# Optimization experiments

Hardware: AMD Instinct MI355X
Metric: run time of the kernel (lower is better)

The kernel has to match this reference:

```python
import jax, jax.numpy as jnp
import numpy as np

N, E, F_IN, H = 10000, 20000, 128, 8
C1, C2 = 512, 256          # per-head channels: head_dim1*8, head_dim2*8
B, OUT = 64, 10            # graphs per batch, output_dim


def _lin(k, fi, fo):
    return (jax.random.normal(k, (fi, fo), jnp.float32) / np.sqrt(fi)).astype(jnp.float32)


def setup_inputs() -> dict:
    key = jax.random.key(0)
    ks = jax.random.split(key, 24)
    inp = {
        "x": jax.random.normal(ks[0], (N, F_IN), jnp.float32),
        "edge_index": jax.random.randint(ks[1], (2, E), 0, N),
        "batch": jnp.sort(jax.random.randint(ks[2], (N,), 0, B)),
        # conv1 (in=F_IN, per-head C1, H heads)
        "Wq1": _lin(ks[3], F_IN, H * C1), "bq1": 0.01 * jax.random.normal(ks[4], (H * C1,)),
        "Wk1": _lin(ks[5], F_IN, H * C1), "bk1": 0.01 * jax.random.normal(ks[6], (H * C1,)),
        "Wv1": _lin(ks[7], F_IN, H * C1), "bv1": 0.01 * jax.random.normal(ks[8], (H * C1,)),
        "Ws1": _lin(ks[9], F_IN, C1), "bs1": 0.01 * jax.random.normal(ks[10], (C1,)),
        # conv2 (in=C1, per-head C2)
        "Wq2": _lin(ks[11], C1, H * C2), "bq2": 0.01 * jax.random.normal(ks[12], (H * C2,)),
        "Wk2": _lin(ks[13], C1, H * C2), "bk2": 0.01 * jax.random.normal(ks[14], (H * C2,)),
        "Wv2": _lin(ks[15], C1, H * C2), "bv2": 0.01 * jax.random.normal(ks[16], (H * C2,)),
        "Ws2": _lin(ks[17], C1, C2), "bs2": 0.01 * jax.random.normal(ks[18], (C2,)),
        # GlobalAttention gate and final fc
        "Wg": _lin(ks[19], C2, 1), "bg": jnp.zeros((1,), jnp.float32),
        "Wf": _lin(ks[20], C2, OUT), "bf": 0.01 * jax.random.normal(ks[21], (OUT,)),
    }
    return inp


def _segment_softmax(alpha, idx, n):
    # numerically-stable softmax over variable-size segments (PyG softmax)
    amax = jax.ops.segment_max(alpha, idx, num_segments=n)
    amax = jnp.where(jnp.isfinite(amax), amax, 0.0)
    e = jnp.exp(alpha - amax[idx])
    denom = jax.ops.segment_sum(e, idx, num_segments=n)
    return e / (denom[idx] + 1e-16)


def _transformer_conv(x, edge_index, Wq, bq, Wk, bk, Wv, bv, Ws, bs, C):
    n = x.shape[0]
    src, dst = edge_index[0], edge_index[1]  # message flows src -> dst
    q = (x @ Wq + bq).reshape(n, H, C)
    k = (x @ Wk + bk).reshape(n, H, C)
    v = (x @ Wv + bv).reshape(n, H, C)
    # per-edge multi-head attention logits [E, H]
    alpha = jnp.einsum('ehc,ehc->eh', q[dst], k[src]) / np.sqrt(C).astype(np.float32)
    a = _segment_softmax(alpha, dst, n)                       # [E, H]
    out = jax.ops.segment_sum(a[:, :, None] * v[src], dst, num_segments=n)  # [N, H, C]
    out = out.mean(axis=1)                                    # concat=False -> head mean
    return out + x @ Ws + bs                                  # root/skip connection


def reference(x, edge_index, batch,
              Wq1, bq1, Wk1, bk1, Wv1, bv1, Ws1, bs1,
              Wq2, bq2, Wk2, bk2, Wv2, bv2, Ws2, bs2,
              Wg, bg, Wf, bf):
    h = jax.nn.elu(_transformer_conv(x, edge_index, Wq1, bq1, Wk1, bk1, Wv1, bv1, Ws1, bs1, C1))
    h = jax.nn.elu(_transformer_conv(h, edge_index, Wq2, bq2, Wk2, bk2, Wv2, bv2, Ws2, bs2, C2))
    # GlobalAttention pooling: gate softmax within each graph, weighted sum
    gate = _segment_softmax((h @ Wg + bg)[:, 0], batch, B)    # [N]
    g = jax.ops.segment_sum(gate[:, None] * h, batch, num_segments=B)  # [B, C2]
    return g @ Wf + bf
```

## Files before the change

### kernel.cpp

```cpp
#include <hip/hip_runtime.h>
#include <math.h>

#define NN 10000
#define NE 20000
#define FIN 128
#define NHEAD 8
#define C1 512
#define C2 256
#define NB 64
#define NOUT 10

typedef _Float16 half8v __attribute__((ext_vector_type(8)));
typedef _Float16 half4v __attribute__((ext_vector_type(4)));
typedef _Float16 half2v __attribute__((ext_vector_type(2)));
typedef float f32x4 __attribute__((ext_vector_type(4)));

template<int VEC> struct VecT;
template<> struct VecT<2> { using T = half2v; };
template<> struct VecT<4> { using T = half4v; };
template<> struct VecT<8> { using T = half8v; };

__device__ __forceinline__ unsigned enc_f(float f) {
    unsigned u = __float_as_uint(f);
    return (u & 0x80000000u) ? ~u : (u | 0x80000000u);
}
__device__ __forceinline__ float dec_f(unsigned e) {
    return (e & 0x80000000u) ? __uint_as_float(e & 0x7fffffffu) : __uint_as_float(~e);
}

__device__ __forceinline__ void gload16(const _Float16* g, _Float16* l) {
    __builtin_amdgcn_global_load_lds(
        (const __attribute__((address_space(1))) unsigned int*)(const void*)g,
        (__attribute__((address_space(3))) unsigned int*)(void*)l, 16, 0, 0);
}

__global__ void cvt_f16(const float* __restrict__ in, _Float16* __restrict__ out, int n) {
    int i = blockIdx.x * blockDim.x + threadIdx.x;
    if (i < n) out[i] = (_Float16)in[i];
}

__global__ void transpose_cvt(const float* __restrict__ W, _Float16* __restrict__ Wt,
                              int K, int N) {
    __shared__ float tile[32][33];
    int n0 = blockIdx.x * 32, k0 = blockIdx.y * 32;
    int tx = threadIdx.x, ty = threadIdx.y;
    for (int j = ty; j < 32; j += 8) tile[j][tx] = W[(size_t)(k0 + j) * N + n0 + tx];
    __syncthreads();
    for (int j = ty; j < 32; j += 8)
        Wt[(size_t)(n0 + j) * K + k0 + tx] = (_Float16)tile[tx][j];
}

__global__ void transpose_stack(const float* __restrict__ Wv, _Float16* __restrict__ Bt,
                                int Cin, int Cout) {
    __shared__ float tile[32][33];
    int h = blockIdx.z;
    int c0 = blockIdx.x * 32, k0 = blockIdx.y * 32;
    int tx = threadIdx.x, ty = threadIdx.y;
    for (int j = ty; j < 32; j += 8)
        tile[j][tx] = Wv[(size_t)(k0 + j) * (NHEAD * Cout) + (size_t)h * Cout + c0 + tx];
    __syncthreads();
    for (int j = ty; j < 32; j += 8)
        Bt[(size_t)(c0 + j) * (NHEAD * Cin) + (size_t)h * Cin + k0 + tx] = (_Float16)tile[tx][j];
}

__global__ void bvmean_k(const float* __restrict__ bv, float* __restrict__ bvm, int C) {
    int c = blockIdx.x * blockDim.x + threadIdx.x;
    if (c >= C) return;
    float s = 0.f;
    #pragma unroll
    for (int h = 0; h < NHEAD; ++h) s += bv[h * C + c];
    bvm[c] = s * (1.0f / NHEAD);
}

__global__ void concat_bias3(const float* __restrict__ a, const float* __restrict__ b,
                             const float* __restrict__ c, float* __restrict__ o) {
    int i = blockIdx.x * blockDim.x + threadIdx.x;
    const int n = NHEAD * C2;
    if (i < n) o[i] = a[i];
    else if (i < 2 * n) o[i] = b[i - n];
    else if (i < 3 * n) o[i] = c[i - 2 * n];
}

__global__ void mstack_k(const _Float16* __restrict__ wtq1, const _Float16* __restrict__ wtk1,
                         _Float16* __restrict__ Mst) {
    int h = blockIdx.z;
    int i = blockIdx.x * 16 + threadIdx.x;
    int j = blockIdx.y * 16 + threadIdx.y;
    float acc = 0.f;
    for (int c = 0; c < C1; ++c)
        acc += (float)wtq1[((size_t)h * C1 + c) * FIN + i] *
               (float)wtk1[((size_t)h * C1 + c) * FIN + j];
    Mst[((size_t)h * FIN + j) * FIN + i] = (_Float16)acc;
}

__global__ void uvprep(const float* __restrict__ Wq1, const float* __restrict__ Wk1,
                       const float* __restrict__ bq1, const float* __restrict__ bk1,
                       float* __restrict__ u, float* __restrict__ v, float* __restrict__ ch) {
    int h = blockIdx.x, i = threadIdx.x;
    float su = 0.f, sv = 0.f;
    for (int c = 0; c < C1; ++c) {
        su += Wq1[(size_t)i * (NHEAD * C1) + h * C1 + c] * bk1[h * C1 + c];
        sv += Wk1[(size_t)i * (NHEAD * C1) + h * C1 + c] * bq1[h * C1 + c];
    }
    u[h * FIN + i] = su;
    v[h * FIN + i] = sv;
    if (i == 0) {
        float s = 0.f;
        for (int c = 0; c < C1; ++c) s += bq1[h * C1 + c] * bk1[h * C1 + c];
        ch[h] = s;
    }
}

__global__ void udvs_k(const _Float16* __restrict__ xb, const float* __restrict__ u,
                       const float* __restrict__ v, const float* __restrict__ ch,
                       float* __restrict__ ud, float* __restrict__ vs) {
    int idx = blockIdx.x * blockDim.x + threadIdx.x;
    if (idx >= NN * NHEAD) return;
    int n = idx >> 3, h = idx & 7;
    float su = ch[h], sv = 0.f;
    for (int i = 0; i < FIN; ++i) {
        float xv = (float)xb[(size_t)n * FIN + i];
        su += xv * u[h * FIN + i];
        sv += xv * v[h * FIN + i];
    }
    ud[idx] = su;
    vs[idx] = sv;
}

template<bool OUT_HALF, bool ACCUM>
__global__ __launch_bounds__(256) void gemm_tn(
    const _Float16* __restrict__ A, const _Float16* __restrict__ Bt,
    const float* __restrict__ bias, void* __restrict__ Cout, int ldc,
    int M, int K)
{
    __shared__ _Float16 As[128 * 32];
    __shared__ _Float16 Bs[128 * 32];
    const int t = threadIdx.x;
    const int m0 = blockIdx.y * 128, n0 = blockIdx.x * 128;
    const int w = t >> 6, lane = t & 63;
    const int wr = w >> 1, wc = w & 1;
    const int r_lo = lane >> 2, slot = lane & 3;

    f32x4 acc[4][4];
    #pragma unroll
    for (int m = 0; m < 4; ++m)
        #pragma unroll
        for (int n = 0; n < 4; ++n)
            #pragma unroll
            for (int j = 0; j < 4; ++j) acc[m][n][j] = 0.f;

    for (int k0 = 0; k0 < K; k0 += 32) {
        #pragma unroll
        for (int i = 0; i < 2; ++i) {
            int chunk = 2 * w + i;
            int row = chunk * 16 + r_lo;
            int gr = m0 + row; gr = gr < M ? gr : M - 1;
            gload16(A + (size_t)gr * K + k0 + slot * 8, &As[chunk * 512]);
            gload16(Bt + (size_t)(n0 + row) * K + k0 + slot * 8, &Bs[chunk * 512]);
        }
        __syncthreads();
        half8v af[4], bf[4];
        #pragma unroll
        for (int m = 0; m < 4; ++m)
            af[m] = *(const half8v*)(&As[(wr * 64 + m * 16 + (lane & 15)) * 32 + (lane >> 4) * 8]);
        #pragma unroll
        for (int n = 0; n < 4; ++n)
            bf[n] = *(const half8v*)(&Bs[(wc * 64 + n * 16 + (lane & 15)) * 32 + (lane >> 4) * 8]);
        #pragma unroll
        for (int m = 0; m < 4; ++m)
            #pragma unroll
            for (int n = 0; n < 4; ++n)
                acc[m][n] = __builtin_amdgcn_mfma_f32_16x16x32_f16(af[m], bf[n], acc[m][n], 0, 0, 0);
        __syncthreads();
    }
    #pragma unroll
    for (int m = 0; m < 4; ++m) {
        int r0 = m0 + wr * 64 + m * 16 + (lane >> 4) * 4;
        #pragma unroll
        for (int n = 0; n < 4; ++n) {
            int col = n0 + wc * 64 + n * 16 + (lane & 15);
            float b = 0.f;
            if (!ACCUM) b = bias[col];
            #pragma unroll
            for (int r = 0; r < 4; ++r) {
                int row = r0 + r;
                if (row < M) {
                    float v = acc[m][n][r] + b;
                    if (ACCUM) v += ((float*)Cout)[(size_t)row * ldc + col];
                    if (OUT_HALF) ((_Float16*)Cout)[(size_t)row * ldc + col] = (_Float16)v;
                    else          ((float*)Cout)[(size_t)row * ldc + col] = v;
                }
            }
        }
    }
}

__global__ void zero_i32(int* __restrict__ p, int n) {
    int i = blockIdx.x * blockDim.x + threadIdx.x;
    if (i < n) p[i] = 0;
}
__global__ void hist_dst(const int* __restrict__ dst, int* __restrict__ deg) {
    int e = blockIdx.x * blockDim.x + threadIdx.x;
    if (e < NE) atomicAdd(&deg[dst[e]], 1);
}
__global__ void scan_deg(const int* __restrict__ deg, int* __restrict__ rowptr,
                         int* __restrict__ cursor, int n) {
    __shared__ int s[256];
    __shared__ int carry;
    int t = threadIdx.x;
    if (t == 0) carry = 0;
    __syncthreads();
    for (int base = 0; base < n; base += 256) {
        int v = (base + t < n) ? deg[base + t] : 0;
        s[t] = v;
        __syncthreads();
        for (int off = 1; off < 256; off <<= 1) {
            int x = (t >= off) ? s[t - off] : 0;
            __syncthreads();
            s[t] += x;
            __syncthreads();
        }
        int excl = carry + s[t] - v;
        if (base + t < n) { rowptr[base + t] = excl; cursor[base + t] = excl; }
        __syncthreads();
        if (t == 255) carry += s[255];
        __syncthreads();
    }
    if (t == 0) rowptr[n] = carry;
}
__global__ void scatter_edges(const int* __restrict__ dst, int* __restrict__ cursor,
                              int* __restrict__ eids) {
    int e = blockIdx.x * blockDim.x + threadIdx.x;
    if (e < NE) {
        int pos = atomicAdd(&cursor[dst[e]], 1);
        eids[pos] = e;
    }
}

__global__ void init_seg(unsigned* __restrict__ amax, float* __restrict__ denom, int n) {
    int i = blockIdx.x * blockDim.x + threadIdx.x;
    if (i < n) { amax[i] = 0x007FFFFFu; denom[i] = 0.f; }
}

__global__ void edge_alpha_lr(const _Float16* __restrict__ T, const _Float16* __restrict__ X,
                              const float* __restrict__ ud, const float* __restrict__ vs,
                              const int* __restrict__ src, const int* __restrict__ dst,
                              float* __restrict__ alpha, unsigned* __restrict__ amaxU,
                              float scale)
{
    int gi = blockIdx.x * blockDim.x + threadIdx.x;
    int e = gi >> 6, lane = threadIdx.x & 63;
    if (e >= NE) return;
    int s = src[e], d = dst[e];
    half2v xv = *(const half2v*)(X + (size_t)s * FIN + lane * 2);
    #pragma unroll
    for (int h = 0; h < NHEAD; ++h) {
        half2v tv = *(const half2v*)(T + ((size_t)d * NHEAD + h) * FIN + lane * 2);
        float sum = (float)tv[0] * (float)xv[0] + (float)tv[1] * (float)xv[1];
        #pragma unroll
        for (int off = 32; off; off >>= 1) sum += __shfl_xor(sum, off);
        if (lane == 0) {
            float al = (sum + ud[(size_t)d * NHEAD + h] + vs[(size_t)s * NHEAD + h]) * scale;
            alpha[(size_t)e * NHEAD + h] = al;
            atomicMax(&amaxU[(size_t)d * NHEAD + h], enc_f(al));
        }
    }
}

template<int C>
__global__ void edge_alpha_f(const _Float16* __restrict__ Q, const _Float16* __restrict__ Kh,
                             int ldq, const int* __restrict__ src, const int* __restrict__ dst,
                             float* __restrict__ alpha, unsigned* __restrict__ amaxU,
                             float scale, int hbase, int G)
{
    constexpr int VEC = C / 64;
    using vecH = typename VecT<VEC>::T;
    int gi = blockIdx.x * blockDim.x + threadIdx.x;
    int e = gi >> 6, lane = threadIdx.x & 63;
    if (e >= NE) return;
    int s = src[e], d = dst[e];
    const _Float16* qp = Q + (size_t)d * ldq + lane * VEC;
    const _Float16* kp = Kh + (size_t)s * ldq + lane * VEC;
    for (int h = 0; h < G; ++h) {
        vecH q = *(const vecH*)(qp + h * C);
        vecH k = *(const vecH*)(kp + h * C);
        float sum = 0.f;
        #pragma unroll
        for (int j = 0; j < VEC; ++j) sum += (float)q[j] * (float)k[j];
        #pragma unroll
        for (int off = 32; off; off >>= 1) sum += __shfl_xor(sum, off);
        if (lane == 0) {
            float al = sum * scale;
            alpha[(size_t)e * NHEAD + hbase + h] = al;
            atomicMax(&amaxU[(size_t)d * NHEAD + hbase + h], enc_f(al));
        }
    }
}

__global__ void edge_expsum(const float* __restrict__ alpha, const int* __restrict__ dst,
                            const unsigned* __restrict__ amaxU,
                            float* __restrict__ ev, float* __restrict__ denom)
{
    int i = blockIdx.x * blockDim.x + threadIdx.x;
    if (i >= NE * NHEAD) return;
    int e = i >> 3, h = i & 7;
    int d = dst[e];
    float ex = expf(alpha[i] - dec_f(amaxU[(size_t)d * NHEAD + h]));
    ev[i] = ex;
    atomicAdd(&denom[(size_t)d * NHEAD + h], ex);
}

template<int C, int G>
__global__ void zaccum(const _Float16* __restrict__ X, const float* __restrict__ ev,
                       const float* __restrict__ denom, const int* __restrict__ rowptr,
                       const int* __restrict__ eids, const int* __restrict__ src,
                       _Float16* __restrict__ Z, int hbase)
{
    constexpr int VEC = C / 64;
    using vecH = typename VecT<VEC>::T;
    int gi = blockIdx.x * blockDim.x + threadIdx.x;
    int n = gi >> 6, lane = threadIdx.x & 63;
    if (n >= NN) return;
    int beg = rowptr[n], end = rowptr[n + 1];
    float rd[G];
    #pragma unroll
    for (int h = 0; h < G; ++h)
        rd[h] = (1.0f / NHEAD) / (denom[(size_t)n * NHEAD + hbase + h] + 1e-16f);
    float acc[G][VEC];
    #pragma unroll
    for (int h = 0; h < G; ++h)
        #pragma unroll
        for (int j = 0; j < VEC; ++j) acc[h][j] = 0.f;
    for (int i = beg; i < end; ++i) {
        int e = eids[i];
        int s = src[e];
        vecH xv = *(const vecH*)(X + (size_t)s * C + lane * VEC);
        #pragma unroll
        for (int h = 0; h < G; ++h) {
            float cf = ev[(size_t)e * NHEAD + hbase + h] * rd[h];
            #pragma unroll
            for (int j = 0; j < VEC; ++j) acc[h][j] += cf * (float)xv[j];
        }
    }
    #pragma unroll
    for (int h = 0; h < G; ++h) {
        vecH o;
        #pragma unroll
        for (int j = 0; j < VEC; ++j) o[j] = (_Float16)acc[h][j];
        *(vecH*)(Z + (size_t)n * (G * C) + (size_t)h * C + lane * VEC) = o;
    }
}

template<int C>
__global__ void node_aggr(const _Float16* __restrict__ V, int ldv,
                          const float* __restrict__ ev, const float* __restrict__ denom,
                          const int* __restrict__ rowptr, const int* __restrict__ eids,
                          const int* __restrict__ src, float* __restrict__ acc,
                          int hbase, int G)
{
    constexpr int VEC = C / 64;
    using vecH = typename VecT<VEC>::T;
    int gi = blockIdx.x * blockDim.x + threadIdx.x;
    int n = gi >> 6, lane = threadIdx.x & 63;
    if (n >= NN) return;
    int beg = rowptr[n], end = rowptr[n + 1];
    float a[VEC];
    #pragma unroll
    for (int j = 0; j < VEC; ++j) a[j] = 0.f;
    for (int h = 0; h < G; ++h) {
        float rd = 1.f / (denom[(size_t)n * NHEAD + hbase + h] + 1e-16f) * (1.f / NHEAD);
        for (int i = beg; i < end; ++i) {
            int e = eids[i];
            int s = src[e];
            float coeff = ev[(size_t)e * NHEAD + hbase + h] * rd;
            vecH v = *(const vecH*)(V + (size_t)s * ldv + h * C + lane * VEC);
            #pragma unroll
            for (int j = 0; j < VEC; ++j) a[j] += coeff * (float)v[j];
        }
    }
    float* ap = acc + (size_t)n * C + lane * VEC;
    #pragma unroll
    for (int j = 0; j < VEC; ++j) ap[j] += a[j];
}

__global__ void elu_k(float* __restrict__ x, int n) {
    int i = blockIdx.x * blockDim.x + threadIdx.x;
    if (i < n) { float v = x[i]; x[i] = v > 0.f ? v : expm1f(v); }
}
__global__ void elu_cvt_bias(const float* __restrict__ in, _Float16* __restrict__ out,
                             const float* __restrict__ bvm, const int* __restrict__ deg,
                             int total) {
    int i = blockIdx.x * blockDim.x + threadIdx.x;
    if (i >= total) return;
    int c = i & (C1 - 1), n = i >> 9;
    float v = in[i] + (deg[n] > 0 ? bvm[c] : 0.f);
    v = v > 0.f ? v : expm1f(v);
    out[i] = (_Float16)v;
}

__global__ __launch_bounds__(256) void pool_fused(
    const float* __restrict__ H2, const float* __restrict__ Wg,
    const float* __restrict__ bg, const int* __restrict__ batch,
    const float* __restrict__ Wf, const float* __restrict__ bf,
    float* __restrict__ glogit, float* __restrict__ out)
{
    const int b = blockIdx.x;
    const int t = threadIdx.x, lane = t & 63, w = t >> 6;
    __shared__ int sbeg, send;
    __shared__ float sred[4];
    if (t == 0) {
        int lo = 0, hi = NN;
        while (lo < hi) { int mid = (lo + hi) >> 1; if (batch[mid] < b) lo = mid + 1; else hi = mid; }
        sbeg = lo;
        hi = NN;
        while (lo < hi) { int mid = (lo + hi) >> 1; if (batch[mid] < b + 1) lo = mid + 1; else hi = mid; }
        send = lo;
    }
    __syncthreads();
    const int beg = sbeg, end = send;
    const float bg0 = bg[0];

    float lmax = -INFINITY;
    for (int n = beg + w; n < end; n += 4) {
        float4 h = ((const float4*)(H2 + (size_t)n * C2))[lane];
        float4 wv = ((const float4*)Wg)[lane];
        float sum = h.x * wv.x + h.y * wv.y + h.z * wv.z + h.w * wv.w;
        #pragma unroll
        for (int off = 32; off; off >>= 1) sum += __shfl_xor(sum, off);
        sum += bg0;
        if (lane == 0) glogit[n] = sum;
        lmax = fmaxf(lmax, sum);
    }
    if (lane == 0) sred[w] = lmax;
    __syncthreads();
    float m = fmaxf(fmaxf(sred[0], sred[1]), fmaxf(sred[2], sred[3]));
    if (!isfinite(m)) m = 0.f;
    __syncthreads();

    float ls = 0.f;
    for (int n = beg + t; n < end; n += 256) {
        float e = expf(glogit[n] - m);
        glogit[n] = e;
        ls += e;
    }
    #pragma unroll
    for (int off = 32; off; off >>= 1) ls += __shfl_xor(ls, off);
    if (lane == 0) sred[w] = ls;
    __syncthreads();
    const float denom = sred[0] + sred[1] + sred[2] + sred[3] + 1e-16f;
    __syncthreads();

    float acc = 0.f;
    for (int n = beg; n < end; ++n)
        acc += glogit[n] * H2[(size_t)n * C2 + t];
    const float gc = acc / denom;

    for (int o = 0; o < NOUT; ++o) {
        float p = gc * Wf[t * NOUT + o];
        #pragma unroll
        for (int off = 32; off; off >>= 1) p += __shfl_xor(p, off);
        __syncthreads();
        if (lane == 0) sred[w] = p;
        __syncthreads();
        if (t == 0) out[b * NOUT + o] = sred[0] + sred[1] + sred[2] + sred[3] + bf[o];
    }
}

extern "C" void kernel_launch(void* const* d_in, const int* in_sizes, int n_in,
                              void* d_out, int out_size, void* d_ws, size_t ws_size,
                              hipStream_t stream) {
    (void)in_sizes; (void)n_in; (void)out_size; (void)ws_size;
    const float* x     = (const float*)d_in[0];
    const int*   ei    = (const int*)  d_in[1];
    const int*   batch = (const int*)  d_in[2];
    const float* Wq1 = (const float*)d_in[3];  const float* bq1 = (const float*)d_in[4];
    const float* Wk1 = (const float*)d_in[5];  const float* bk1 = (const float*)d_in[6];
    const float* Wv1 = (const float*)d_in[7];  const float* bv1 = (const float*)d_in[8];
    const float* Ws1 = (const float*)d_in[9];  const float* bs1 = (const float*)d_in[10];
    const float* Wq2 = (const float*)d_in[11]; const float* bq2 = (const float*)d_in[12];
    const float* Wk2 = (const float*)d_in[13]; const float* bk2 = (const float*)d_in[14];
    const float* Wv2 = (const float*)d_in[15]; const float* bv2 = (const float*)d_in[16];
    const float* Ws2 = (const float*)d_in[17]; const float* bs2 = (const float*)d_in[18];
    const float* Wg  = (const float*)d_in[19]; const float* bg  = (const float*)d_in[20];
    const float* Wf  = (const float*)d_in[21]; const float* bf  = (const float*)d_in[22];

    const int* src = ei;
    const int* dst = ei + NE;

    char* base = (char*)d_ws;
    size_t off = 0;
    auto alloc = [&](size_t bytes) -> char* {
        char* p = base + off;
        off = (off + bytes + 255) & ~(size_t)255;
        return p;
    };
    _Float16* xb    = (_Float16*)alloc((size_t)NN * FIN * 2);
    _Float16* wtq1  = (_Float16*)alloc((size_t)NHEAD * C1 * FIN * 2);
    _Float16* wtk1  = (_Float16*)alloc((size_t)NHEAD * C1 * FIN * 2);
    _Float16* bvs1  = (_Float16*)alloc((size_t)C1 * NHEAD * FIN * 2);
    _Float16* wts1  = (_Float16*)alloc((size_t)C1 * FIN * 2);
    _Float16* wqkv2 = (_Float16*)alloc((size_t)3 * NHEAD * C2 * C1 * 2);
    _Float16* wts2  = (_Float16*)alloc((size_t)C2 * C1 * 2);
    _Float16* Mst   = (_Float16*)alloc((size_t)NHEAD * FIN * FIN * 2);
    float* uvecs = (float*)alloc((size_t)NHEAD * FIN * 4);
    float* vvecs = (float*)alloc((size_t)NHEAD * FIN * 4);
    float* chd   = (float*)alloc((size_t)NHEAD * 4);
    float* ud    = (float*)alloc((size_t)NN * NHEAD * 4);
    float* vs    = (float*)alloc((size_t)NN * NHEAD * 4);
    float* zbias = (float*)alloc((size_t)NHEAD * FIN * 4);
    float* bqkv2 = (float*)alloc((size_t)3 * NHEAD * C2 * 4);
    float* acc1  = (float*)alloc((size_t)NN * C1 * 4);
    _Float16* h1b = (_Float16*)alloc((size_t)NN * C1 * 2);
    float* alpha = (float*)alloc((size_t)NE * NHEAD * 4);
    float* ev    = (float*)alloc((size_t)NE * NHEAD * 4);
    unsigned* amaxU = (unsigned*)alloc((size_t)NN * NHEAD * 4);
    float* denom = (float*)alloc((size_t)NN * NHEAD * 4);
    int* deg    = (int*)alloc((size_t)NN * 4);
    int* rowptr = (int*)alloc((size_t)(NN + 1) * 4);
    int* cursor = (int*)alloc((size_t)NN * 4);
    int* eids   = (int*)alloc((size_t)NE * 4);
    float* bvm1 = (float*)alloc((size_t)C1 * 4);
    _Float16* Tbuf   = (_Float16*)alloc((size_t)NN * NHEAD * FIN * 2);
    _Float16* QKVbuf = (_Float16*)alloc((size_t)NN * 3 * NHEAD * C2 * 2);
    _Float16* Zbuf = QKVbuf;
    float* acc2 = acc1;
    const int LDQKV = 3 * NHEAD * C2;

    const dim3 blk(256);
    const float sc1 = 1.0f / sqrtf((float)C1);
    const float sc2 = 1.0f / sqrtf((float)C2);
    const int edge_blocks = (NE * 64) / 256;
    const int node_blocks = (NN * 64) / 256;
    const int gy = (NN + 127) / 128;

    cvt_f16<<<((size_t)NN * FIN + 255) / 256, blk, 0, stream>>>(x, xb, NN * FIN);
    {
        dim3 tb(32, 8);
        transpose_cvt<<<dim3(NHEAD * C1 / 32, FIN / 32), tb, 0, stream>>>(Wq1, wtq1, FIN, NHEAD * C1);
        transpose_cvt<<<dim3(NHEAD * C1 / 32, FIN / 32), tb, 0, stream>>>(Wk1, wtk1, FIN, NHEAD * C1);
        transpose_stack<<<dim3(C1 / 32, FIN / 32, NHEAD), tb, 0, stream>>>(Wv1, bvs1, FIN, C1);
        transpose_cvt<<<dim3(C1 / 32, FIN / 32),         tb, 0, stream>>>(Ws1, wts1, FIN, C1);
        transpose_cvt<<<dim3(NHEAD * C2 / 32, C1 / 32),  tb, 0, stream>>>(Wq2, wqkv2, C1, NHEAD * C2);
        transpose_cvt<<<dim3(NHEAD * C2 / 32, C1 / 32),  tb, 0, stream>>>(
            Wk2, wqkv2 + (size_t)NHEAD * C2 * C1, C1, NHEAD * C2);
        transpose_cvt<<<dim3(NHEAD * C2 / 32, C1 / 32),  tb, 0, stream>>>(
            Wv2, wqkv2 + (size_t)2 * NHEAD * C2 * C1, C1, NHEAD * C2);
        transpose_cvt<<<dim3(C2 / 32, C1 / 32),          tb, 0, stream>>>(Ws2, wts2, C1, C2);
    }
    bvmean_k<<<(C1 + 255) / 256, blk, 0, stream>>>(bv1, bvm1, C1);
    mstack_k<<<dim3(FIN / 16, FIN / 16, NHEAD), dim3(16, 16), 0, stream>>>(wtq1, wtk1, Mst);
    uvprep<<<NHEAD, FIN, 0, stream>>>(Wq1, Wk1, bq1, bk1, uvecs, vvecs, chd);
    udvs_k<<<(NN * NHEAD + 255) / 256, blk, 0, stream>>>(xb, uvecs, vvecs, chd, ud, vs);
    zero_i32<<<(NHEAD * FIN + 255) / 256, blk, 0, stream>>>((int*)zbias, NHEAD * FIN);
    concat_bias3<<<(3 * NHEAD * C2 + 255) / 256, blk, 0, stream>>>(bq2, bk2, bv2, bqkv2);

    zero_i32<<<(NN + 255) / 256, blk, 0, stream>>>(deg, NN);
    hist_dst<<<(NE + 255) / 256, blk, 0, stream>>>(dst, deg);
    scan_deg<<<1, blk, 0, stream>>>(deg, rowptr, cursor, NN);
    scatter_edges<<<(NE + 255) / 256, blk, 0, stream>>>(dst, cursor, eids);

    gemm_tn<true, false><<<dim3(NHEAD * FIN / 128, gy), blk, 0, stream>>>(
        xb, Mst, zbias, Tbuf, NHEAD * FIN, NN, FIN);
    init_seg<<<(NN * NHEAD + 255) / 256, blk, 0, stream>>>(amaxU, denom, NN * NHEAD);
    edge_alpha_lr<<<edge_blocks, blk, 0, stream>>>(Tbuf, xb, ud, vs, src, dst,
                                                   alpha, amaxU, sc1);
    edge_expsum<<<(NE * NHEAD + 255) / 256, blk, 0, stream>>>(alpha, dst, amaxU, ev, denom);
    gemm_tn<false, false><<<dim3(C1 / 128, gy), blk, 0, stream>>>(
        xb, wts1, bs1, acc1, C1, NN, FIN);
    zaccum<FIN, NHEAD><<<node_blocks, blk, 0, stream>>>(xb, ev, denom, rowptr, eids, src,
                                                        Zbuf, 0);
    gemm_tn<false, true><<<dim3(C1 / 128, gy), blk, 0, stream>>>(
        Zbuf, bvs1, nullptr, acc1, C1, NN, NHEAD * FIN);
    elu_cvt_bias<<<((size_t)NN * C1 + 255) / 256, blk, 0, stream>>>(
        acc1, h1b, bvm1, deg, NN * C1);

    gemm_tn<false, false><<<dim3(C2 / 128, gy), blk, 0, stream>>>(
        h1b, wts2, bs2, acc2, C2, NN, C1);
    init_seg<<<(NN * NHEAD + 255) / 256, blk, 0, stream>>>(amaxU, denom, NN * NHEAD);
    gemm_tn<true, false><<<dim3(LDQKV / 128, gy), blk, 0, stream>>>(
        h1b, wqkv2, bqkv2, QKVbuf, LDQKV, NN, C1);
    edge_alpha_f<C2><<<edge_blocks, blk, 0, stream>>>(
        QKVbuf, QKVbuf + NHEAD * C2, LDQKV, src, dst, alpha, amaxU, sc2, 0, NHEAD);
    edge_expsum<<<(NE * NHEAD + 255) / 256, blk, 0, stream>>>(alpha, dst, amaxU, ev, denom);
    node_aggr<C2><<<node_blocks, blk, 0, stream>>>(
        QKVbuf + 2 * NHEAD * C2, LDQKV, ev, denom, rowptr, eids, src, acc2, 0, NHEAD);
    elu_k<<<((size_t)NN * C2 + 255) / 256, blk, 0, stream>>>(acc2, NN * C2);

    pool_fused<<<NB, blk, 0, stream>>>(acc2, Wg, bg, batch, Wf, bf, alpha, (float*)d_out);
}
```

Before: 656.2 us.

## Merge skip GEMMs into QK/QKV GEMMs and add ILP to edge kernels

Concatenates the skip-connection weights onto the attention projection weights, so each layer runs one GEMM over the shared input. A new dual-output epilogue writes half-precision attention columns and fp32 skip columns to separate buffers. Layer-2 edge-logit and node-aggregation kernels now load all heads' vectors up front and iterate edges once with all heads unrolled, rather than looping per head. This removes two kernel launches and re-reads of the input, and adds memory-level parallelism, at the cost of more register pressure.

```diff
diff --git a/kernel.cpp b/kernel.cpp
--- a/kernel.cpp
+++ b/kernel.cpp
@@ -72,13 +72,19 @@
     bvm[c] = s * (1.0f / NHEAD);
 }
 
-__global__ void concat_bias3(const float* __restrict__ a, const float* __restrict__ b,
-                             const float* __restrict__ c, float* __restrict__ o) {
+__global__ void bcat1_k(const float* __restrict__ bs1, float* __restrict__ o) {
+    int i = blockIdx.x * blockDim.x + threadIdx.x;
+    if (i < NHEAD * FIN + C1) o[i] = (i < NHEAD * FIN) ? 0.f : bs1[i - NHEAD * FIN];
+}
+__global__ void bcat2_k(const float* __restrict__ bq2, const float* __restrict__ bk2,
+                        const float* __restrict__ bv2, const float* __restrict__ bs2,
+                        float* __restrict__ o) {
     int i = blockIdx.x * blockDim.x + threadIdx.x;
     const int n = NHEAD * C2;
-    if (i < n) o[i] = a[i];
-    else if (i < 2 * n) o[i] = b[i - n];
-    else if (i < 3 * n) o[i] = c[i - 2 * n];
+    if (i < n) o[i] = bq2[i];
+    else if (i < 2 * n) o[i] = bk2[i - n];
+    else if (i < 3 * n) o[i] = bv2[i - 2 * n];
+    else if (i < 3 * n + C2) o[i] = bs2[i - 3 * n];
 }
 
 __global__ void mstack_k(const _Float16* __restrict__ wtq1, const _Float16* __restrict__ wtk1,
@@ -127,52 +133,53 @@
     vs[idx] = sv;
 }
 
+#define GEMM_BODY                                                                   \
+    __shared__ _Float16 As[128 * 32];                                               \
+    __shared__ _Float16 Bs[128 * 32];                                               \
+    const int t = threadIdx.x;                                                      \
+    const int m0 = blockIdx.y * 128, n0 = blockIdx.x * 128;                         \
+    const int w = t >> 6, lane = t & 63;                                            \
+    const int wr = w >> 1, wc = w & 1;                                              \
+    const int r_lo = lane >> 2, slot = lane & 3;                                    \
+    f32x4 acc[4][4];                                                                \
+    _Pragma("unroll")                                                               \
+    for (int m = 0; m < 4; ++m)                                                     \
+        _Pragma("unroll")                                                           \
+        for (int n = 0; n < 4; ++n)                                                 \
+            _Pragma("unroll")                                                       \
+            for (int j = 0; j < 4; ++j) acc[m][n][j] = 0.f;                         \
+    for (int k0 = 0; k0 < K; k0 += 32) {                                            \
+        _Pragma("unroll")                                                           \
+        for (int i = 0; i < 2; ++i) {                                               \
+            int chunk = 2 * w + i;                                                  \
+            int row = chunk * 16 + r_lo;                                            \
+            int gr = m0 + row; gr = gr < M ? gr : M - 1;                            \
+            gload16(A + (size_t)gr * K + k0 + slot * 8, &As[chunk * 512]);          \
+            gload16(Bt + (size_t)(n0 + row) * K + k0 + slot * 8, &Bs[chunk * 512]); \
+        }                                                                           \
+        __syncthreads();                                                            \
+        half8v af[4], bf[4];                                                        \
+        _Pragma("unroll")                                                           \
+        for (int m = 0; m < 4; ++m)                                                 \
+            af[m] = *(const half8v*)(&As[(wr * 64 + m * 16 + (lane & 15)) * 32 + (lane >> 4) * 8]); \
+        _Pragma("unroll")                                                           \
+        for (int n = 0; n < 4; ++n)                                                 \
+            bf[n] = *(const half8v*)(&Bs[(wc * 64 + n * 16 + (lane & 15)) * 32 + (lane >> 4) * 8]); \
+        _Pragma("unroll")                                                           \
+        for (int m = 0; m < 4; ++m)                                                 \
+            _Pragma("unroll")                                                       \
+            for (int n = 0; n < 4; ++n)                                             \
+                acc[m][n] = __builtin_amdgcn_mfma_f32_16x16x32_f16(af[m], bf[n], acc[m][n], 0, 0, 0); \
+        __syncthreads();                                                            \
+    }
+
 template<bool OUT_HALF, bool ACCUM>
 __global__ __launch_bounds__(256) void gemm_tn(
     const _Float16* __restrict__ A, const _Float16* __restrict__ Bt,
     const float* __restrict__ bias, void* __restrict__ Cout, int ldc,
     int M, int K)
 {
-    __shared__ _Float16 As[128 * 32];
-    __shared__ _Float16 Bs[128 * 32];
-    const int t = threadIdx.x;
-    const int m0 = blockIdx.y * 128, n0 = blockIdx.x * 128;
-    const int w = t >> 6, lane = t & 63;
-    const int wr = w >> 1, wc = w & 1;
-    const int r_lo = lane >> 2, slot = lane & 3;
-
-    f32x4 acc[4][4];
-    #pragma unroll
-    for (int m = 0; m < 4; ++m)
-        #pragma unroll
-        for (int n = 0; n < 4; ++n)
-            #pragma unroll
-            for (int j = 0; j < 4; ++j) acc[m][n][j] = 0.f;
-
-    for (int k0 = 0; k0 < K; k0 += 32) {
-        #pragma unroll
-        for (int i = 0; i < 2; ++i) {
-            int chunk = 2 * w + i;
-            int row = chunk * 16 + r_lo;
-            int gr = m0 + row; gr = gr < M ? gr : M - 1;
-            gload16(A + (size_t)gr * K + k0 + slot * 8, &As[chunk * 512]);
-            gload16(Bt + (size_t)(n0 + row) * K + k0 + slot * 8, &Bs[chunk * 512]);
-        }
-        __syncthreads();
-        half8v af[4], bf[4];
-        #pragma unroll
-        for (int m = 0; m < 4; ++m)
-            af[m] = *(const half8v*)(&As[(wr * 64 + m * 16 + (lane & 15)) * 32 + (lane >> 4) * 8]);
-        #pragma unroll
-        for (int n = 0; n < 4; ++n)
-            bf[n] = *(const half8v*)(&Bs[(wc * 64 + n * 16 + (lane & 15)) * 32 + (lane >> 4) * 8]);
-        #pragma unroll
-        for (int m = 0; m < 4; ++m)
-            #pragma unroll
-            for (int n = 0; n < 4; ++n)
-                acc[m][n] = __builtin_amdgcn_mfma_f32_16x16x32_f16(af[m], bf[n], acc[m][n], 0, 0, 0);
-        __syncthreads();
-    }
+    GEMM_BODY
     #pragma unroll
     for (int m = 0; m < 4; ++m) {
         int r0 = m0 + wr * 64 + m * 16 + (lane >> 4) * 4;
@@ -195,6 +202,32 @@
     }
 }
 
+__global__ __launch_bounds__(256) void gemm_dual(
+    const _Float16* __restrict__ A, const _Float16* __restrict__ Bt,
+    const float* __restrict__ bias, _Float16* __restrict__ out16, int ld16,
+    float* __restrict__ out32, int ld32, int NSPLIT, int M, int K)
+{
+    GEMM_BODY
+    #pragma unroll
+    for (int m = 0; m < 4; ++m) {
+        int r0 = m0 + wr * 64 + m * 16 + (lane >> 4) * 4;
+        #pragma unroll
+        for (int n = 0; n < 4; ++n) {
+            int col = n0 + wc * 64 + n * 16 + (lane & 15);
+            float b = bias[col];
+            #pragma unroll
+            for (int r = 0; r < 4; ++r) {
+                int row = r0 + r;
+                if (row < M) {
+                    float v = acc[m][n][r] + b;
+                    if (col < NSPLIT) out16[(size_t)row * ld16 + col] = (_Float16)v;
+                    else              out32[(size_t)row * ld32 + (col - NSPLIT)] = v;
+                }
+            }
+        }
+    }
+}
+
 __global__ void zero_i32(int* __restrict__ p, int n) {
     int i = blockIdx.x * blockDim.x + threadIdx.x;
     if (i < n) p[i] = 0;
@@ -267,11 +300,11 @@
     }
 }
 
-template<int C>
-__global__ void edge_alpha_f(const _Float16* __restrict__ Q, const _Float16* __restrict__ Kh,
-                             int ldq, const int* __restrict__ src, const int* __restrict__ dst,
-                             float* __restrict__ alpha, unsigned* __restrict__ amaxU,
-                             float scale, int hbase, int G)
+template<int C, int G>
+__global__ void edge_alpha_fu(const _Float16* __restrict__ Q, const _Float16* __restrict__ Kh,
+                              int ldq, const int* __restrict__ src, const int* __restrict__ dst,
+                              float* __restrict__ alpha, unsigned* __restrict__ amaxU,
+                              float scale)
 {
     constexpr int VEC = C / 64;
     using vecH = typename VecT<VEC>::T;
@@ -281,18 +314,23 @@
     int s = src[e], d = dst[e];
     const _Float16* qp = Q + (size_t)d * ldq + lane * VEC;
     const _Float16* kp = Kh + (size_t)s * ldq + lane * VEC;
+    vecH q[G], k[G];
+    #pragma unroll
     for (int h = 0; h < G; ++h) {
-        vecH q = *(const vecH*)(qp + h * C);
-        vecH k = *(const vecH*)(kp + h * C);
+        q[h] = *(const vecH*)(qp + h * C);
+        k[h] = *(const vecH*)(kp + h * C);
+    }
+    #pragma unroll
+    for (int h = 0; h < G; ++h) {
         float sum = 0.f;
         #pragma unroll
-        for (int j = 0; j < VEC; ++j) sum += (float)q[j] * (float)k[j];
+        for (int j = 0; j < VEC; ++j) sum += (float)q[h][j] * (float)k[h][j];
         #pragma unroll
         for (int off = 32; off; off >>= 1) sum += __shfl_xor(sum, off);
         if (lane == 0) {
             float al = sum * scale;
-            alpha[(size_t)e * NHEAD + hbase + h] = al;
-            atomicMax(&amaxU[(size_t)d * NHEAD + hbase + h], enc_f(al));
+            alpha[(size_t)e * NHEAD + h] = al;
+            atomicMax(&amaxU[(size_t)d * NHEAD + h], enc_f(al));
         }
     }
 }
@@ -351,12 +389,11 @@
     }
 }
 
-template<int C>
-__global__ void node_aggr(const _Float16* __restrict__ V, int ldv,
-                          const float* __restrict__ ev, const float* __restrict__ denom,
-                          const int* __restrict__ rowptr, const int* __restrict__ eids,
-                          const int* __restrict__ src, float* __restrict__ acc,
-                          int hbase, int G)
+template<int C, int G>
+__global__ void node_aggr_ilp(const _Float16* __restrict__ V, int ldv,
+                              const float* __restrict__ ev, const float* __restrict__ denom,
+                              const int* __restrict__ rowptr, const int* __restrict__ eids,
+                              const int* __restrict__ src, float* __restrict__ acc)
 {
     constexpr int VEC = C / 64;
     using vecH = typename VecT<VEC>::T;
@@ -364,19 +401,27 @@
     int n = gi >> 6, lane = threadIdx.x & 63;
     if (n >= NN) return;
     int beg = rowptr[n], end = rowptr[n + 1];
+    float rd[G];
+    #pragma unroll
+    for (int h = 0; h < G; ++h)
+        rd[h] = (1.0f / NHEAD) / (denom[(size_t)n * NHEAD + h] + 1e-16f);
     float a[VEC];
     #pragma unroll
     for (int j = 0; j < VEC; ++j) a[j] = 0.f;
-    for (int h = 0; h < G; ++h) {
-        float rd = 1.f / (denom[(size_t)n * NHEAD + hbase + h] + 1e-16f) * (1.f / NHEAD);
-        for (int i = beg; i < end; ++i) {
-            int e = eids[i];
-            int s = src[e];
-            float coeff = ev[(size_t)e * NHEAD + hbase + h] * rd;
-            vecH v = *(const vecH*)(V + (size_t)s * ldv + h * C + lane * VEC);
+    for (int i = beg; i < end; ++i) {
+        int e = eids[i];
+        int s = src[e];
+        float cf[G];
+        #pragma unroll
+        for (int h = 0; h < G; ++h) cf[h] = ev[(size_t)e * NHEAD + h] * rd[h];
+        vecH v[G];
+        #pragma unroll
+        for (int h = 0; h < G; ++h)
+            v[h] = *(const vecH*)(V + (size_t)s * ldv + h * C + lane * VEC);
+        #pragma unroll
+        for (int h = 0; h < G; ++h)
             #pragma unroll
-            for (int j = 0; j < VEC; ++j) a[j] += coeff * (float)v[j];
-        }
+            for (int j = 0; j < VEC; ++j) a[j] += cf[h] * (float)v[h][j];
     }
     float* ap = acc + (size_t)n * C + lane * VEC;
     #pragma unroll
@@ -498,17 +543,15 @@
     _Float16* wtq1  = (_Float16*)alloc((size_t)NHEAD * C1 * FIN * 2);
     _Float16* wtk1  = (_Float16*)alloc((size_t)NHEAD * C1 * FIN * 2);
     _Float16* bvs1  = (_Float16*)alloc((size_t)C1 * NHEAD * FIN * 2);
-    _Float16* wts1  = (_Float16*)alloc((size_t)C1 * FIN * 2);
-    _Float16* wqkv2 = (_Float16*)alloc((size_t)3 * NHEAD * C2 * C1 * 2);
-    _Float16* wts2  = (_Float16*)alloc((size_t)C2 * C1 * 2);
-    _Float16* Mst   = (_Float16*)alloc((size_t)NHEAD * FIN * FIN * 2);
+    _Float16* wcat1 = (_Float16*)alloc((size_t)(NHEAD * FIN + C1) * FIN * 2);
+    _Float16* wcat2 = (_Float16*)alloc((size_t)(3 * NHEAD * C2 + C2) * C1 * 2);
     float* uvecs = (float*)alloc((size_t)NHEAD * FIN * 4);
     float* vvecs = (float*)alloc((size_t)NHEAD * FIN * 4);
     float* chd   = (float*)alloc((size_t)NHEAD * 4);
     float* ud    = (float*)alloc((size_t)NN * NHEAD * 4);
     float* vs    = (float*)alloc((size_t)NN * NHEAD * 4);
-    float* zbias = (float*)alloc((size_t)NHEAD * FIN * 4);
-    float* bqkv2 = (float*)alloc((size_t)3 * NHEAD * C2 * 4);
+    float* bcat1 = (float*)alloc((size_t)(NHEAD * FIN + C1) * 4);
+    float* bcat2 = (float*)alloc((size_t)(3 * NHEAD * C2 + C2) * 4);
     float* acc1  = (float*)alloc((size_t)NN * C1 * 4);
     _Float16* h1b = (_Float16*)alloc((size_t)NN * C1 * 2);
     float* alpha = (float*)alloc((size_t)NE * NHEAD * 4);
@@ -526,6 +569,13 @@
     float* acc2 = acc1;
     const int LDQKV = 3 * NHEAD * C2;
 
+    _Float16* Mst  = wcat1;
+    _Float16* wts1 = wcat1 + (size_t)NHEAD * FIN * FIN;
+    _Float16* wq2t = wcat2;
+    _Float16* wk2t = wcat2 + (size_t)NHEAD * C2 * C1;
+    _Float16* wv2t = wcat2 + (size_t)2 * NHEAD * C2 * C1;
+    _Float16* ws2t = wcat2 + (size_t)3 * NHEAD * C2 * C1;
+
     const dim3 blk(256);
     const float sc1 = 1.0f / sqrtf((float)C1);
     const float sc2 = 1.0f / sqrtf((float)C2);
@@ -540,33 +590,29 @@
         transpose_cvt<<<dim3(NHEAD * C1 / 32, FIN / 32), tb, 0, stream>>>(Wk1, wtk1, FIN, NHEAD * C1);
         transpose_stack<<<dim3(C1 / 32, FIN / 32, NHEAD), tb, 0, stream>>>(Wv1, bvs1, FIN, C1);
         transpose_cvt<<<dim3(C1 / 32, FIN / 32),         tb, 0, stream>>>(Ws1, wts1, FIN, C1);
-        transpose_cvt<<<dim3(NHEAD * C2 / 32, C1 / 32),  tb, 0, stream>>>(Wq2, wqkv2, C1, NHEAD * C2);
-        transpose_cvt<<<dim3(NHEAD * C2 / 32, C1 / 32),  tb, 0, stream>>>(
-            Wk2, wqkv2 + (size_t)NHEAD * C2 * C1, C1, NHEAD * C2);
-        transpose_cvt<<<dim3(NHEAD * C2 / 32, C1 / 32),  tb, 0, stream>>>(
-            Wv2, wqkv2 + (size_t)2 * NHEAD * C2 * C1, C1, NHEAD * C2);
-        transpose_cvt<<<dim3(C2 / 32, C1 / 32),          tb, 0, stream>>>(Ws2, wts2, C1, C2);
+        transpose_cvt<<<dim3(NHEAD * C2 / 32, C1 / 32),  tb, 0, stream>>>(Wq2, wq2t, C1, NHEAD * C2);
+        transpose_cvt<<<dim3(NHEAD * C2 / 32, C1 / 32),  tb, 0, stream>>>(Wk2, wk2t, C1, NHEAD * C2);
+        transpose_cvt<<<dim3(NHEAD * C2 / 32, C1 / 32),  tb, 0, stream>>>(Wv2, wv2t, C1, NHEAD * C2);
+        transpose_cvt<<<dim3(C2 / 32, C1 / 32),          tb, 0, stream>>>(Ws2, ws2t, C1, C2);
     }
     bvmean_k<<<(C1 + 255) / 256, blk, 0, stream>>>(bv1, bvm1, C1);
     mstack_k<<<dim3(FIN / 16, FIN / 16, NHEAD), dim3(16, 16), 0, stream>>>(wtq1, wtk1, Mst);
     uvprep<<<NHEAD, FIN, 0, stream>>>(Wq1, Wk1, bq1, bk1, uvecs, vvecs, chd);
     udvs_k<<<(NN * NHEAD + 255) / 256, blk, 0, stream>>>(xb, uvecs, vvecs, chd, ud, vs);
-    zero_i32<<<(NHEAD * FIN + 255) / 256, blk, 0, stream>>>((int*)zbias, NHEAD * FIN);
-    concat_bias3<<<(3 * NHEAD * C2 + 255) / 256, blk, 0, stream>>>(bq2, bk2, bv2, bqkv2);
+    bcat1_k<<<(NHEAD * FIN + C1 + 255) / 256, blk, 0, stream>>>(bs1, bcat1);
+    bcat2_k<<<(3 * NHEAD * C2 + C2 + 255) / 256, blk, 0, stream>>>(bq2, bk2, bv2, bs2, bcat2);
 
     zero_i32<<<(NN + 255) / 256, blk, 0, stream>>>(deg, NN);
     hist_dst<<<(NE + 255) / 256, blk, 0, stream>>>(dst, deg);
     scan_deg<<<1, blk, 0, stream>>>(deg, rowptr, cursor, NN);
     scatter_edges<<<(NE + 255) / 256, blk, 0, stream>>>(dst, cursor, eids);
 
-    gemm_tn<true, false><<<dim3(NHEAD * FIN / 128, gy), blk, 0, stream>>>(
-        xb, Mst, zbias, Tbuf, NHEAD * FIN, NN, FIN);
+    gemm_dual<<<dim3((NHEAD * FIN + C1) / 128, gy), blk, 0, stream>>>(
+        xb, wcat1, bcat1, Tbuf, NHEAD * FIN, acc1, C1, NHEAD * FIN, NN, FIN);
     init_seg<<<(NN * NHEAD + 255) / 256, blk, 0, stream>>>(amaxU, denom, NN * NHEAD);
     edge_alpha_lr<<<edge_blocks, blk, 0, stream>>>(Tbuf, xb, ud, vs, src, dst,
                                                    alpha, amaxU, sc1);
     edge_expsum<<<(NE * NHEAD + 255) / 256, blk, 0, stream>>>(alpha, dst, amaxU, ev, denom);
-    gemm_tn<false, false><<<dim3(C1 / 128, gy), blk, 0, stream>>>(
-        xb, wts1, bs1, acc1, C1, NN, FIN);
     zaccum<FIN, NHEAD><<<node_blocks, blk, 0, stream>>>(xb, ev, denom, rowptr, eids, src,
                                                         Zbuf, 0);
     gemm_tn<false, true><<<dim3(C1 / 128, gy), blk, 0, stream>>>(
@@ -574,16 +620,14 @@
     elu_cvt_bias<<<((size_t)NN * C1 + 255) / 256, blk, 0, stream>>>(
         acc1, h1b, bvm1, deg, NN * C1);
 
-    gemm_tn<false, false><<<dim3(C2 / 128, gy), blk, 0, stream>>>(
-        h1b, wts2, bs2, acc2, C2, NN, C1);
     init_seg<<<(NN * NHEAD + 255) / 256, blk, 0, stream>>>(amaxU, denom, NN * NHEAD);
-    gemm_tn<true, false><<<dim3(LDQKV / 128, gy), blk, 0, stream>>>(
-        h1b, wqkv2, bqkv2, QKVbuf, LDQKV, NN, C1);
-    edge_alpha_f<C2><<<edge_blocks, blk, 0, stream>>>(
-        QKVbuf, QKVbuf + NHEAD * C2, LDQKV, src, dst, alpha, amaxU, sc2, 0, NHEAD);
+    gemm_dual<<<dim3((LDQKV + C2) / 128, gy), blk, 0, stream>>>(
+        h1b, wcat2, bcat2, QKVbuf, LDQKV, acc2, C2, LDQKV, NN, C1);
+    edge_alpha_fu<C2, NHEAD><<<edge_blocks, blk, 0, stream>>>(
+        QKVbuf, QKVbuf + NHEAD * C2, LDQKV, src, dst, alpha, amaxU, sc2);
     edge_expsum<<<(NE * NHEAD + 255) / 256, blk, 0, stream>>>(alpha, dst, amaxU, ev, denom);
-    node_aggr<C2><<<node_blocks, blk, 0, stream>>>(
-        QKVbuf + 2 * NHEAD * C2, LDQKV, ev, denom, rowptr, eids, src, acc2, 0, NHEAD);
+    node_aggr_ilp<C2, NHEAD><<<node_blocks, blk, 0, stream>>>(
+        QKVbuf + 2 * NHEAD * C2, LDQKV, ev, denom, rowptr, eids, src, acc2);
     elu_k<<<((size_t)NN * C2 + 255) / 256, blk, 0, stream>>>(acc2, NN * C2);
 
     pool_fused<<<NB, blk, 0, stream>>>(acc2, Wg, bg, batch, Wf, bf, alpha, (float*)d_out);
```

After: 617.6 us. 5.9% less time.
